# Kernel optimization log

Measured on AMD Instinct MI355X. Metric: run time of the kernel, lower is better.

## Reference

```python
import jax, jax.numpy as jnp
import numpy as np

B = 256; M = 6; H = 448; INC = 448; EMB = 32; NHEAD = 8; DFF = 2048
OBS = 20; HOR = 30
D = EMB + 4 * NHEAD + INC      # transformer d_model = 512 (requires INC == hidden_dim)
LBUF = OBS + HOR               # 50-token buffer; index 49 is written but never read
HD = D // NHEAD
FUS_IN = D + 7 + INC           # fusion layer input = 71 + 2*hidden_dim


def _ln(x, g, b):
    mu = x.mean(-1, keepdims=True)
    var = ((x - mu) ** 2).mean(-1, keepdims=True)
    return (x - mu) * jax.lax.rsqrt(var + 1e-5) * g + b


def setup_inputs() -> dict:
    key = jax.random.key(0)
    ks = jax.random.split(key, 16)
    s = jnp.float32(0.02)
    n = lambda i, shp: jax.random.normal(ks[i], shp, dtype=jnp.float32)
    return {
        "feat_in": n(0, (B, 1, INC)),
        "loc_in": n(1, (B, M, 2)),
        "obs_trajs": n(2, (OBS, B, 2)),
        "W_emb": n(3, (2, EMB)) * s, "b_emb": jnp.zeros((EMB,)),
        "W_qkv": n(4, (D, 3 * D)) * s, "b_qkv": jnp.zeros((3 * D,)),
        "W_o": n(5, (D, D)) * s, "b_o": jnp.zeros((D,)),
        "W_ff1": n(6, (D, DFF)) * s, "b_ff1": jnp.zeros((DFF,)),
        "W_ff2": n(7, (DFF, D)) * s, "b_ff2": jnp.zeros((D,)),
        "ln1_g": jnp.ones((D,)), "ln1_b": jnp.zeros((D,)),
        "ln2_g": jnp.ones((D,)), "ln2_b": jnp.zeros((D,)),
        "W_fus": n(8, (FUS_IN, H)) * s, "b_fus": jnp.zeros((H,)),
        "W_out": n(9, (H, 2)) * s, "b_out": jnp.zeros((2,)),
    }


def reference(feat_in, loc_in, obs_trajs, W_emb, b_emb, W_qkv, b_qkv, W_o, b_o,
              W_ff1, b_ff1, W_ff2, b_ff2, ln1_g, ln1_b, ln2_g, ln2_b,
              W_fus, b_fus, W_out, b_out):
    feat = feat_in[:, 0]                                     # [B, INC]
    emb_obs = jax.nn.relu(obs_trajs @ W_emb + b_emb)         # [OBS, B, EMB]
    pos0 = jnp.zeros((LBUF, B, 2), feat.dtype).at[:OBS].set(obs_trajs)
    emb0 = jnp.zeros((LBUF, B, EMB), feat.dtype).at[:OBS].set(emb_obs)
    idxs = jnp.arange(OBS, OBS + HOR)
    scale = 1.0 / jnp.sqrt(jnp.float32(HD))
    rep = NHEAD // 2

    def run_sample(goal):                                    # goal: [B, 2]
        def step(carry, frame_idx):
            pos, emb = carry
            last = pos[frame_idx - 1]                        # [B, 2]
            dist = goal - last
            tcol = jnp.zeros((B, 1), feat.dtype) + frame_idx
            # order matches torch.cat: (emb, goal, last, dist, time, feat)
            extras = jnp.concatenate([jnp.tile(goal, (1, rep)), jnp.tile(last, (1, rep)),
                                      jnp.tile(dist, (1, rep)), jnp.tile(tcol, (1, NHEAD))], -1)
            x = jnp.concatenate([emb,
                                 jnp.broadcast_to(extras, (LBUF, B, 4 * NHEAD)),
                                 jnp.broadcast_to(feat, (LBUF, B, INC))], -1)   # [LBUF, B, D]
            qkv = x @ W_qkv + b_qkv
            q, k, v = jnp.split(qkv, 3, axis=-1)
            qh = q[frame_idx - 1].reshape(B, NHEAD, HD)      # only last query needed
            kh = k.reshape(LBUF, B, NHEAD, HD)
            vh = v.reshape(LBUF, B, NHEAD, HD)
            scores = jnp.einsum('bhd,lbhd->bhl', qh, kh) * scale
            valid = jnp.arange(LBUF) < frame_idx             # tokens 0..frame_idx-1 exist
            scores = jnp.where(valid[None, None, :], scores, -1e9)
            attn = jax.nn.softmax(scores, axis=-1)
            ctx = jnp.einsum('bhl,lbhd->bhd', attn, vh).reshape(B, D)
            a = ctx @ W_o + b_o
            x_last = x[frame_idx - 1]
            h1 = _ln(x_last + a, ln1_g, ln1_b)               # post-LN encoder layer (eval, no dropout)
            ff = jax.nn.relu(h1 @ W_ff1 + b_ff1) @ W_ff2 + b_ff2
            h2 = _ln(h1 + ff, ln2_g, ln2_b)
            fus = jnp.concatenate([h2, last, goal, dist, tcol, feat], -1)       # [B, FUS_IN]
            out = (fus @ W_fus + b_fus) @ W_out + b_out                         # [B, 2]
            pos = pos.at[frame_idx].set(out)
            emb = emb.at[frame_idx].set(jax.nn.relu(out @ W_emb + b_emb))
            return (pos, emb), out
        _, ys = jax.lax.scan(step, (pos0, emb0), idxs)
        return ys                                            # [HOR, B, 2]

    ys = jax.vmap(run_sample, in_axes=1)(loc_in)             # [M, HOR, B, 2]
    return ys.transpose(2, 0, 1, 3).reshape(B, M, HOR * 2)
```

## Files before the change

kernel.cpp:

```cpp
#include <hip/hip_runtime.h>
#include <math.h>

#define B_   256
#define N_   1536
#define OBS_ 20
#define HOR_ 30

typedef __bf16 bf16;
typedef bf16  bf16x8 __attribute__((ext_vector_type(8)));
typedef float f32x4  __attribute__((ext_vector_type(4)));

__global__ __launch_bounds__(256) void gemm_k(
    const float* __restrict__ A, int lda,
    const float* __restrict__ Bw, int ldb,
    float* __restrict__ C, bf16* __restrict__ Cb, int ldc,
    int K, const float* __restrict__ colBias)
{
    __shared__ float As[16][68];
    __shared__ float Bs[16][68];
    const int tid = threadIdx.x;
    const int tx = tid & 15, ty = tid >> 4;
    const int n0 = blockIdx.y * 64, j0 = blockIdx.x * 64;
    float acc[4][4] = {};
    const int a_kk = tid & 15, a_nn0 = tid >> 4;
    const int b_jj = tid & 63, b_kk0 = tid >> 6;
    for (int k0 = 0; k0 < K; k0 += 16) {
#pragma unroll
        for (int i = 0; i < 4; i++) {
            int nn = a_nn0 + 16 * i;
            As[a_kk][nn] = (k0 + a_kk < K) ? A[(size_t)(n0 + nn) * lda + k0 + a_kk] : 0.f;
        }
#pragma unroll
        for (int i = 0; i < 4; i++) {
            int kk = b_kk0 + 4 * i;
            Bs[kk][b_jj] = (k0 + kk < K) ? Bw[(size_t)(k0 + kk) * ldb + j0 + b_jj] : 0.f;
        }
        __syncthreads();
#pragma unroll
        for (int kk = 0; kk < 16; kk++) {
            float4 av = *(const float4*)&As[kk][ty * 4];
            float4 bv = *(const float4*)&Bs[kk][tx * 4];
            float aa[4] = {av.x, av.y, av.z, av.w};
            float bb[4] = {bv.x, bv.y, bv.z, bv.w};
#pragma unroll
            for (int i = 0; i < 4; i++)
#pragma unroll
                for (int j = 0; j < 4; j++) acc[i][j] += aa[i] * bb[j];
        }
        __syncthreads();
    }
#pragma unroll
    for (int i = 0; i < 4; i++) {
        int n = n0 + ty * 4 + i;
#pragma unroll
        for (int j = 0; j < 4; j++) {
            int jj = j0 + tx * 4 + j;
            float v = acc[i][j];
            if (colBias) v += colBias[jj];
            if (C)  C[(size_t)n * ldc + jj] = v;
            if (Cb) Cb[(size_t)n * ldc + jj] = (bf16)v;
        }
    }
}

__global__ void pack_k(const float* __restrict__ srcF, const bf16* __restrict__ srcB,
                       int srcRows, int KC, int J, int lds, bf16* __restrict__ dst)
{
    int idx = blockIdx.x * 256 + threadIdx.x;
    int total = (J / 16) * KC * 64;
    if (idx >= total) return;
    int lane = idx & 63;
    int kc = (idx >> 6) % KC;
    int jg = idx / (64 * KC);
    int k0 = kc * 32 + (lane >> 4) * 8;
    int col = jg * 16 + (lane & 15);
    bf16x8 v;
#pragma unroll
    for (int i = 0; i < 8; i++) {
        int r = k0 + i;
        float x = 0.f;
        if (r < srcRows) x = srcF ? srcF[(size_t)r * lds + col] : (float)srcB[(size_t)r * lds + col];
        v[i] = (bf16)x;
    }
    *(bf16x8*)&dst[(size_t)idx * 8] = v;
}

template<int KC>
__global__ __launch_bounds__(256) void fgemm_k(
    const bf16* __restrict__ A, int lda,
    const bf16* __restrict__ Bp,
    float* __restrict__ C, bf16* __restrict__ Cb, int ldc,
    const float* __restrict__ colBias,
    const float* __restrict__ rowMat, int ldRm,
    int doRelu)
{
    const int n0 = blockIdx.y * 32;
    const int j0g = blockIdx.x * 4;
    const int tid = threadIdx.x;
    const int w = tid >> 6, lane = tid & 63;
    const int quad = lane >> 4, m15 = lane & 15;
    const int r0 = (w & 1) * 16;
    const int cg = (w >> 1) * 2;
    const bf16* Arow = &A[(size_t)(n0 + r0 + m15) * lda + quad * 8];
    const bf16* B0 = &Bp[((size_t)(j0g + cg) * KC * 64 + lane) * 8];
    const bf16* B1 = &Bp[((size_t)(j0g + cg + 1) * KC * 64 + lane) * 8];
    f32x4 acc0 = {}, acc1 = {};
#pragma unroll 8
    for (int kc = 0; kc < KC; kc++) {
        bf16x8 af = *(const bf16x8*)&Arow[kc * 32];
        bf16x8 b0 = *(const bf16x8*)&B0[(size_t)kc * 512];
        bf16x8 b1 = *(const bf16x8*)&B1[(size_t)kc * 512];
        acc0 = __builtin_amdgcn_mfma_f32_16x16x32_bf16(af, b0, acc0, 0, 0, 0);
        acc1 = __builtin_amdgcn_mfma_f32_16x16x32_bf16(af, b1, acc1, 0, 0, 0);
    }
#pragma unroll
    for (int g = 0; g < 2; g++) {
        f32x4 a = g ? acc1 : acc0;
        int j = (j0g + cg + g) * 16 + m15;
        float cb = colBias ? colBias[j] : 0.f;
#pragma unroll
        for (int r = 0; r < 4; r++) {
            int n = n0 + r0 + quad * 4 + r;
            float v = a[r] + cb;
            if (rowMat) v += rowMat[(size_t)(n / 6) * ldRm + j];
            if (doRelu) v = fmaxf(v, 0.f);
            if (C)  C[(size_t)n * ldc + j] = v;
            if (Cb) Cb[(size_t)n * ldc + j] = (bf16)v;
        }
    }
}

__global__ __launch_bounds__(256) void emb_obs_k(
    const float* __restrict__ obs, const float* __restrict__ Wemb,
    const float* __restrict__ bemb, float* __restrict__ emb_obs)
{
    int tid = blockIdx.x * 256 + threadIdx.x;
    if (tid >= OBS_ * B_ * 32) return;
    int r = tid >> 5, e = tid & 31;
    float v = obs[r * 2] * Wemb[e] + obs[r * 2 + 1] * Wemb[32 + e] + bemb[e];
    emb_obs[tid] = fmaxf(v, 0.f);
}

__global__ __launch_bounds__(256) void weff_k(
    const float* __restrict__ Wqkv, const float* __restrict__ bqkv,
    float* __restrict__ Weff)
{
    __shared__ float qrow[512];
    const int r = blockIdx.x;
    const int t = threadIdx.x;
    for (int j = t; j < 512; j += 256)
        qrow[j] = (r < 512) ? Wqkv[(size_t)r * 1536 + j] : bqkv[j];
    __syncthreads();
    const int h = t >> 5, c = t & 31;
    float acc = 0.f;
#pragma unroll 8
    for (int d = 0; d < 64; d++)
        acc += qrow[h * 64 + d] * Wqkv[(size_t)c * 1536 + 512 + h * 64 + d];
    Weff[(size_t)r * 256 + t] = acc;
}

__global__ __launch_bounds__(256) void wov_k(
    const float* __restrict__ Wqkv, const float* __restrict__ Wo,
    bf16* __restrict__ WovCat)
{
    __shared__ float vrow[64];
    const int row = blockIdx.x;
    const int h = row >> 5, c = row & 31;
    const int t = threadIdx.x;
    if (t < 64) vrow[t] = Wqkv[(size_t)c * 1536 + 1024 + h * 64 + t];
    __syncthreads();
    for (int j = t; j < 512; j += 256) {
        float acc = 0.f;
#pragma unroll 8
        for (int d = 0; d < 64; d++)
            acc += vrow[d] * Wo[(size_t)(h * 64 + d) * 512 + j];
        WovCat[(size_t)row * 512 + j] = (bf16)acc;
    }
}

__global__ __launch_bounds__(256) void attn_k(
    const float* __restrict__ qp, const float* __restrict__ emb_obs,
    const float* __restrict__ emb_gen, bf16* __restrict__ ecA1b, int t)
{
    __shared__ float qp_s[256];
    __shared__ float emb_s[50 * 33];
    __shared__ float at_s[4][64];
    const int n = blockIdx.x, b = n / 6, tid = threadIdx.x;
    qp_s[tid] = qp[(size_t)n * 256 + tid];
    for (int idx = tid; idx < t * 32; idx += 256) {
        int l = idx >> 5, c = idx & 31;
        emb_s[l * 33 + c] = (l < OBS_) ? emb_obs[((size_t)l * B_ + b) * 32 + c]
                                       : emb_gen[((size_t)(l - OBS_) * N_ + n) * 32 + c];
    }
    __syncthreads();
    const int w = tid >> 6, lane = tid & 63;
#pragma unroll
    for (int hh = 0; hh < 2; hh++) {
        const int h = w * 2 + hh;
        float sc = -1e30f;
        if (lane < t) {
            float s_ = 0.f;
#pragma unroll 8
            for (int c = 0; c < 32; c++) s_ += emb_s[lane * 33 + c] * qp_s[h * 32 + c];
            sc = s_ * 0.125f;
        }
        float mx = sc;
#pragma unroll
        for (int o = 32; o > 0; o >>= 1) mx = fmaxf(mx, __shfl_xor(mx, o, 64));
        float e = (lane < t) ? __expf(sc - mx) : 0.f;
        float sm = e;
#pragma unroll
        for (int o = 32; o > 0; o >>= 1) sm += __shfl_xor(sm, o, 64);
        at_s[w][lane] = e / sm;
        if (lane < 32) {
            float ec = 0.f;
            for (int l = 0; l < t; l++) ec += at_s[w][l] * emb_s[l * 33 + lane];
            ecA1b[(size_t)n * 288 + h * 32 + lane] = (bf16)ec;
        }
    }
}

__global__ __launch_bounds__(256) void ln1_k(
    const float* __restrict__ a, const float* __restrict__ A1f,
    const float* __restrict__ feat, const float* __restrict__ g,
    const float* __restrict__ bt, float* __restrict__ h1f, bf16* __restrict__ h1b)
{
    __shared__ float red[8];
    const int n = blockIdx.x, b = n / 6, tid = threadIdx.x;
    float r[2]; float s = 0.f, sq = 0.f;
#pragma unroll
    for (int i = 0; i < 2; i++) {
        int j = tid + i * 256;
        float x = (j < 64) ? A1f[(size_t)n * 64 + j] : feat[(size_t)b * 448 + (j - 64)];
        float v = a[(size_t)n * 512 + j] + x;
        r[i] = v; s += v; sq += v * v;
    }
#pragma unroll
    for (int o = 32; o > 0; o >>= 1) { s += __shfl_xor(s, o, 64); sq += __shfl_xor(sq, o, 64); }
    int w = tid >> 6, lane = tid & 63;
    if (lane == 0) { red[w] = s; red[4 + w] = sq; }
    __syncthreads();
    s  = red[0] + red[1] + red[2] + red[3];
    sq = red[4] + red[5] + red[6] + red[7];
    float mu = s * (1.f / 512.f);
    float var = sq * (1.f / 512.f) - mu * mu;
    float rs = rsqrtf(var + 1e-5f);
#pragma unroll
    for (int i = 0; i < 2; i++) {
        int j = tid + i * 256;
        float v = (r[i] - mu) * rs * g[j] + bt[j];
        h1f[(size_t)n * 512 + j] = v;
        h1b[(size_t)n * 512 + j] = (bf16)v;
    }
}

__global__ __launch_bounds__(256) void ln2_k(
    const float* __restrict__ h1, const float* __restrict__ ff,
    const float* __restrict__ g, const float* __restrict__ bt,
    const float* __restrict__ small5, bf16* __restrict__ h2p)
{
    __shared__ float red[8];
    const int n = blockIdx.x, tid = threadIdx.x;
    float r[2]; float s = 0.f, sq = 0.f;
#pragma unroll
    for (int i = 0; i < 2; i++) {
        int j = tid + i * 256;
        float v = h1[(size_t)n * 512 + j] + ff[(size_t)n * 512 + j];
        r[i] = v; s += v; sq += v * v;
    }
#pragma unroll
    for (int o = 32; o > 0; o >>= 1) { s += __shfl_xor(s, o, 64); sq += __shfl_xor(sq, o, 64); }
    int w = tid >> 6, lane = tid & 63;
    if (lane == 0) { red[w] = s; red[4 + w] = sq; }
    __syncthreads();
    s  = red[0] + red[1] + red[2] + red[3];
    sq = red[4] + red[5] + red[6] + red[7];
    float mu = s * (1.f / 512.f);
    float var = sq * (1.f / 512.f) - mu * mu;
    float rs = rsqrtf(var + 1e-5f);
#pragma unroll
    for (int i = 0; i < 2; i++) {
        int j = tid + i * 256;
        h2p[(size_t)n * 544 + j] = (bf16)((r[i] - mu) * rs * g[j] + bt[j]);
    }
    if (tid < 7)  h2p[(size_t)n * 544 + 512 + tid] = (bf16)small5[n * 8 + tid];
    if (tid < 25) h2p[(size_t)n * 544 + 519 + tid] = (bf16)0.f;
}

__device__ __forceinline__ void next_state(
    int n, int b, int t, float o0, float o1, float g0, float g1, float tc,
    const float* Wemb, const float* bemb, const float* Weff, const float* featqp,
    float* emb_dst, float* A1f, bf16* ecA1b, float* small5, float* qp, float* A1s)
{
    float d0 = g0 - o0, d1 = g1 - o1;
    if (t < 32) {
        float e = fmaxf(o0 * Wemb[t] + o1 * Wemb[32 + t] + bemb[t], 0.f);
        if (emb_dst) emb_dst[t] = e;
        A1s[t] = e;
    } else if (t < 64) {
        int c = t - 32;
        float v;
        if      (c < 8)  v = (c & 1) ? g1 : g0;
        else if (c < 16) v = (c & 1) ? o1 : o0;
        else if (c < 24) v = (c & 1) ? d1 : d0;
        else             v = tc;
        A1s[t] = v;
    }
    if (t < 7) {
        float v2 = (t==0)?o0:(t==1)?o1:(t==2)?g0:(t==3)?g1:(t==4)?d0:(t==5)?d1:tc;
        small5[n * 8 + t] = v2;
    }
    __syncthreads();
    if (t < 64) {
        A1f[(size_t)n * 64 + t] = A1s[t];
        if (t >= 32) ecA1b[(size_t)n * 288 + 256 + (t - 32)] = (bf16)A1s[t];
    }
    float acc = featqp[(size_t)b * 256 + t];
#pragma unroll 8
    for (int k = 0; k < 64; k++) acc += A1s[k] * Weff[k * 256 + t];
    qp[(size_t)n * 256 + t] = acc;
}

__global__ __launch_bounds__(256) void init_k(
    const float* __restrict__ obs, const float* __restrict__ emb_obs,
    const float* __restrict__ loc, const float* __restrict__ Weff,
    const float* __restrict__ featqp,
    float* __restrict__ A1f, bf16* __restrict__ ecA1b,
    float* __restrict__ small5, float* __restrict__ qp)
{
    __shared__ float A1s[64];
    const int n = blockIdx.x, b = n / 6, m = n % 6, t = threadIdx.x;
    float o0 = obs[(19 * B_ + b) * 2], o1 = obs[(19 * B_ + b) * 2 + 1];
    float g0 = loc[b * 12 + m * 2], g1 = loc[b * 12 + m * 2 + 1];
    if (t < 32) {
        A1s[t] = emb_obs[((size_t)19 * B_ + b) * 32 + t];
    } else if (t < 64) {
        int c = t - 32; float d0 = g0 - o0, d1 = g1 - o1; float tc = 20.f;
        float v;
        if      (c < 8)  v = (c & 1) ? g1 : g0;
        else if (c < 16) v = (c & 1) ? o1 : o0;
        else if (c < 24) v = (c & 1) ? d1 : d0;
        else             v = tc;
        A1s[t] = v;
    }
    if (t < 7) {
        float d0 = g0 - o0, d1 = g1 - o1; float tc = 20.f;
        float v2 = (t==0)?o0:(t==1)?o1:(t==2)?g0:(t==3)?g1:(t==4)?d0:(t==5)?d1:tc;
        small5[n * 8 + t] = v2;
    }
    __syncthreads();
    if (t < 64) {
        A1f[(size_t)n * 64 + t] = A1s[t];
        if (t >= 32) ecA1b[(size_t)n * 288 + 256 + (t - 32)] = (bf16)A1s[t];
    }
    float acc = featqp[(size_t)b * 256 + t];
#pragma unroll 8
    for (int k = 0; k < 64; k++) acc += A1s[k] * Weff[k * 256 + t];
    qp[(size_t)n * 256 + t] = acc;
}

__global__ __launch_bounds__(256) void finish_k(
    const float* __restrict__ fusv, const float* __restrict__ Wout,
    const float* __restrict__ bout, const float* __restrict__ Wemb,
    const float* __restrict__ bemb, const float* __restrict__ loc,
    const float* __restrict__ Weff, const float* __restrict__ featqp,
    float* __restrict__ dout, float* __restrict__ emb_gen,
    float* __restrict__ A1f, bf16* __restrict__ ecA1b,
    float* __restrict__ small5, float* __restrict__ qp, int s)
{
    __shared__ float red[8];
    __shared__ float osh[2];
    __shared__ float A1s[64];
    const int n = blockIdx.x, b = n / 6, m = n % 6, t = threadIdx.x;
    float f0 = fusv[(size_t)n * 448 + t];
    float p0 = f0 * Wout[t * 2];
    float p1 = f0 * Wout[t * 2 + 1];
    if (t < 192) {
        float f1 = fusv[(size_t)n * 448 + 256 + t];
        p0 += f1 * Wout[(256 + t) * 2];
        p1 += f1 * Wout[(256 + t) * 2 + 1];
    }
#pragma unroll
    for (int o = 32; o > 0; o >>= 1) { p0 += __shfl_xor(p0, o, 64); p1 += __shfl_xor(p1, o, 64); }
    int w = t >> 6, lane = t & 63;
    if (lane == 0) { red[w] = p0; red[4 + w] = p1; }
    __syncthreads();
    if (t == 0) {
        float o0 = red[0] + red[1] + red[2] + red[3] + bout[0];
        float o1 = red[4] + red[5] + red[6] + red[7] + bout[1];
        osh[0] = o0; osh[1] = o1;
        dout[(size_t)b * 360 + m * 60 + s * 2]     = o0;
        dout[(size_t)b * 360 + m * 60 + s * 2 + 1] = o1;
    }
    __syncthreads();
    float o0 = osh[0], o1 = osh[1];
    float g0 = loc[b * 12 + m * 2], g1 = loc[b * 12 + m * 2 + 1];
    next_state(n, b, t, o0, o1, g0, g1, (float)(OBS_ + s + 1),
               Wemb, bemb, Weff, featqp,
               &emb_gen[((size_t)s * N_ + n) * 32], A1f, ecA1b, small5, qp, A1s);
}

extern "C" void kernel_launch(void* const* d_in, const int* in_sizes, int n_in,
                              void* d_out_, int out_size, void* d_ws, size_t ws_size,
                              hipStream_t stream) {
    (void)in_sizes; (void)n_in; (void)out_size; (void)ws_size;
    const float* feat  = (const float*)d_in[0];
    const float* loc   = (const float*)d_in[1];
    const float* obs   = (const float*)d_in[2];
    const float* W_emb = (const float*)d_in[3];
    const float* b_emb = (const float*)d_in[4];
    const float* W_qkv = (const float*)d_in[5];
    const float* b_qkv = (const float*)d_in[6];
    const float* W_o   = (const float*)d_in[7];
    const float* b_o   = (const float*)d_in[8];
    const float* W_ff1 = (const float*)d_in[9];
    const float* b_ff1 = (const float*)d_in[10];
    const float* W_ff2 = (const float*)d_in[11];
    const float* b_ff2 = (const float*)d_in[12];
    const float* ln1_g = (const float*)d_in[13];
    const float* ln1_b = (const float*)d_in[14];
    const float* ln2_g = (const float*)d_in[15];
    const float* ln2_b = (const float*)d_in[16];
    const float* W_fus = (const float*)d_in[17];
    const float* b_fus = (const float*)d_in[18];
    const float* W_out = (const float*)d_in[19];
    const float* b_out = (const float*)d_in[20];
    float* dout = (float*)d_out_;

    float* ws = (float*)d_ws;
    float* Weff     = ws; ws += 513 * 256;
    float* featqp   = ws; ws += 256 * 256;
    float* featv    = ws; ws += 256 * 512;
    float* featvO   = ws; ws += 256 * 512;
    float* feat_fus = ws; ws += 256 * 448;
    float* emb_obs  = ws; ws += OBS_ * B_ * 32;
    float* emb_gen  = ws; ws += HOR_ * N_ * 32;
    float* qp       = ws; ws += (size_t)N_ * 256;
    float* A1f      = ws; ws += (size_t)N_ * 64;
    float* small5   = ws; ws += (size_t)N_ * 8;
    float* h1f      = ws; ws += (size_t)N_ * 512;
    float* aF       = ws; ws += (size_t)N_ * 512;
    float* ffB      = ws; ws += (size_t)N_ * 512;
    float* fusv     = ws; ws += (size_t)N_ * 448;
    bf16* WovCat = (bf16*)ws; ws += (320 * 512) / 2;
    bf16* BpA    = (bf16*)ws; ws += (32 * 9 * 512) / 2;
    bf16* BpF1   = (bf16*)ws; ws += (128 * 16 * 512) / 2;
    bf16* BpF2   = (bf16*)ws; ws += (32 * 64 * 512) / 2;
    bf16* BpFus  = (bf16*)ws; ws += (28 * 17 * 512) / 2;
    bf16* ecA1b  = (bf16*)ws; ws += ((size_t)N_ * 288) / 2;
    bf16* h1b    = (bf16*)ws; ws += ((size_t)N_ * 512) / 2;
    bf16* f1b    = (bf16*)ws; ws += ((size_t)N_ * 2048) / 2;
    bf16* h2p    = (bf16*)ws; ws += ((size_t)N_ * 544) / 2;

    emb_obs_k<<<dim3(640), dim3(256), 0, stream>>>(obs, W_emb, b_emb, emb_obs);
    weff_k<<<dim3(513), dim3(256), 0, stream>>>(W_qkv, b_qkv, Weff);
    gemm_k<<<dim3(4, 4), dim3(256), 0, stream>>>(feat, 448, Weff + 64 * 256, 256,
        featqp, nullptr, 256, 448, Weff + 512 * 256);
    wov_k<<<dim3(256), dim3(256), 0, stream>>>(W_qkv, W_o, WovCat);
    gemm_k<<<dim3(8, 4), dim3(256), 0, stream>>>(feat, 448, W_qkv + 64 * 1536 + 1024, 1536,
        featv, nullptr, 512, 448, b_qkv + 1024);
    gemm_k<<<dim3(8, 4), dim3(256), 0, stream>>>(featv, 512, W_o, 512,
        featvO, nullptr, 512, 512, b_o);
    gemm_k<<<dim3(8, 1), dim3(256), 0, stream>>>(W_qkv + 32 * 1536 + 1024, 1536, W_o, 512,
        featv, WovCat + 256 * 512, 512, 512, nullptr);
    gemm_k<<<dim3(7, 4), dim3(256), 0, stream>>>(feat, 448, W_fus + 519 * 448, 448,
        feat_fus, nullptr, 448, 448, b_fus);
    pack_k<<<dim3(72),  dim3(256), 0, stream>>>(nullptr, WovCat, 288, 9,  512,  512,  BpA);
    pack_k<<<dim3(512), dim3(256), 0, stream>>>(W_ff1, nullptr, 512, 16, 2048, 2048, BpF1);
    pack_k<<<dim3(512), dim3(256), 0, stream>>>(W_ff2, nullptr, 2048, 64, 512, 512,  BpF2);
    pack_k<<<dim3(120), dim3(256), 0, stream>>>(W_fus, nullptr, 519, 17, 448,  448,  BpFus);
    init_k<<<dim3(N_), dim3(256), 0, stream>>>(obs, emb_obs, loc, Weff, featqp,
        A1f, ecA1b, small5, qp);

    for (int s = 0; s < HOR_; s++) {
        attn_k<<<dim3(N_), dim3(256), 0, stream>>>(qp, emb_obs, emb_gen, ecA1b, OBS_ + s);
        fgemm_k<9><<<dim3(8, 48), dim3(256), 0, stream>>>(ecA1b, 288, BpA,
            aF, nullptr, 512, nullptr, featvO, 512, 0);
        ln1_k<<<dim3(N_), dim3(256), 0, stream>>>(aF, A1f, feat, ln1_g, ln1_b, h1f, h1b);
        fgemm_k<16><<<dim3(32, 48), dim3(256), 0, stream>>>(h1b, 512, BpF1,
            nullptr, f1b, 2048, b_ff1, nullptr, 0, 1);
        fgemm_k<64><<<dim3(8, 48), dim3(256), 0, stream>>>(f1b, 2048, BpF2,
            ffB, nullptr, 512, b_ff2, nullptr, 0, 0);
        ln2_k<<<dim3(N_), dim3(256), 0, stream>>>(h1f, ffB, ln2_g, ln2_b, small5, h2p);
        fgemm_k<17><<<dim3(7, 48), dim3(256), 0, stream>>>(h2p, 544, BpFus,
            fusv, nullptr, 448, nullptr, feat_fus, 448, 0);
        finish_k<<<dim3(N_), dim3(256), 0, stream>>>(fusv, W_out, b_out, W_emb, b_emb,
            loc, Weff, featqp, dout, emb_gen, A1f, ecA1b, small5, qp, s);
    }
}
```

Before: 2.938 ms.

## Fuse layernorms into neighbouring MFMA GEMMs and residual adds into epilogues

```diff
diff --git a/kernel.cpp b/kernel.cpp
--- a/kernel.cpp
+++ b/kernel.cpp
@@ -9,6 +9,10 @@
 typedef __bf16 bf16;
 typedef bf16  bf16x8 __attribute__((ext_vector_type(8)));
 typedef float f32x4  __attribute__((ext_vector_type(4)));
+
+__device__ __forceinline__ f32x4 MF(bf16x8 a, bf16x8 b, f32x4 c) {
+    return __builtin_amdgcn_mfma_f32_16x16x32_bf16(a, b, c, 0, 0, 0);
+}
 
 __global__ __launch_bounds__(256) void gemm_k(
     const float* __restrict__ A, int lda,
@@ -85,51 +89,6 @@
     *(bf16x8*)&dst[(size_t)idx * 8] = v;
 }
 
-template<int KC>
-__global__ __launch_bounds__(256) void fgemm_k(
-    const bf16* __restrict__ A, int lda,
-    const bf16* __restrict__ Bp,
-    float* __restrict__ C, bf16* __restrict__ Cb, int ldc,
-    const float* __restrict__ colBias,
-    const float* __restrict__ rowMat, int ldRm,
-    int doRelu)
-{
-    const int n0 = blockIdx.y * 32;
-    const int j0g = blockIdx.x * 4;
-    const int tid = threadIdx.x;
-    const int w = tid >> 6, lane = tid & 63;
-    const int quad = lane >> 4, m15 = lane & 15;
-    const int r0 = (w & 1) * 16;
-    const int cg = (w >> 1) * 2;
-    const bf16* Arow = &A[(size_t)(n0 + r0 + m15) * lda + quad * 8];
-    const bf16* B0 = &Bp[((size_t)(j0g + cg) * KC * 64 + lane) * 8];
-    const bf16* B1 = &Bp[((size_t)(j0g + cg + 1) * KC * 64 + lane) * 8];
-    f32x4 acc0 = {}, acc1 = {};
-#pragma unroll 8
-    for (int kc = 0; kc < KC; kc++) {
-        bf16x8 af = *(const bf16x8*)&Arow[kc * 32];
-        bf16x8 b0 = *(const bf16x8*)&B0[(size_t)kc * 512];
-        bf16x8 b1 = *(const bf16x8*)&B1[(size_t)kc * 512];
-        acc0 = __builtin_amdgcn_mfma_f32_16x16x32_bf16(af, b0, acc0, 0, 0, 0);
-        acc1 = __builtin_amdgcn_mfma_f32_16x16x32_bf16(af, b1, acc1, 0, 0, 0);
-    }
-#pragma unroll
-    for (int g = 0; g < 2; g++) {
-        f32x4 a = g ? acc1 : acc0;
-        int j = (j0g + cg + g) * 16 + m15;
-        float cb = colBias ? colBias[j] : 0.f;
-#pragma unroll
-        for (int r = 0; r < 4; r++) {
-            int n = n0 + r0 + quad * 4 + r;
-            float v = a[r] + cb;
-            if (rowMat) v += rowMat[(size_t)(n / 6) * ldRm + j];
-            if (doRelu) v = fmaxf(v, 0.f);
-            if (C)  C[(size_t)n * ldc + j] = v;
-            if (Cb) Cb[(size_t)n * ldc + j] = (bf16)v;
-        }
-    }
-}
-
 __global__ __launch_bounds__(256) void emb_obs_k(
     const float* __restrict__ obs, const float* __restrict__ Wemb,
     const float* __restrict__ bemb, float* __restrict__ emb_obs)
@@ -176,149 +135,6 @@
             acc += vrow[d] * Wo[(size_t)(h * 64 + d) * 512 + j];
         WovCat[(size_t)row * 512 + j] = (bf16)acc;
     }
-}
-
-__global__ __launch_bounds__(256) void attn_k(
-    const float* __restrict__ qp, const float* __restrict__ emb_obs,
-    const float* __restrict__ emb_gen, bf16* __restrict__ ecA1b, int t)
-{
-    __shared__ float qp_s[256];
-    __shared__ float emb_s[50 * 33];
-    __shared__ float at_s[4][64];
-    const int n = blockIdx.x, b = n / 6, tid = threadIdx.x;
-    qp_s[tid] = qp[(size_t)n * 256 + tid];
-    for (int idx = tid; idx < t * 32; idx += 256) {
-        int l = idx >> 5, c = idx & 31;
-        emb_s[l * 33 + c] = (l < OBS_) ? emb_obs[((size_t)l * B_ + b) * 32 + c]
-                                       : emb_gen[((size_t)(l - OBS_) * N_ + n) * 32 + c];
-    }
-    __syncthreads();
-    const int w = tid >> 6, lane = tid & 63;
-#pragma unroll
-    for (int hh = 0; hh < 2; hh++) {
-        const int h = w * 2 + hh;
-        float sc = -1e30f;
-        if (lane < t) {
-            float s_ = 0.f;
-#pragma unroll 8
-            for (int c = 0; c < 32; c++) s_ += emb_s[lane * 33 + c] * qp_s[h * 32 + c];
-            sc = s_ * 0.125f;
-        }
-        float mx = sc;
-#pragma unroll
-        for (int o = 32; o > 0; o >>= 1) mx = fmaxf(mx, __shfl_xor(mx, o, 64));
-        float e = (lane < t) ? __expf(sc - mx) : 0.f;
-        float sm = e;
-#pragma unroll
-        for (int o = 32; o > 0; o >>= 1) sm += __shfl_xor(sm, o, 64);
-        at_s[w][lane] = e / sm;
-        if (lane < 32) {
-            float ec = 0.f;
-            for (int l = 0; l < t; l++) ec += at_s[w][l] * emb_s[l * 33 + lane];
-            ecA1b[(size_t)n * 288 + h * 32 + lane] = (bf16)ec;
-        }
-    }
-}
-
-__global__ __launch_bounds__(256) void ln1_k(
-    const float* __restrict__ a, const float* __restrict__ A1f,
-    const float* __restrict__ feat, const float* __restrict__ g,
-    const float* __restrict__ bt, float* __restrict__ h1f, bf16* __restrict__ h1b)
-{
-    __shared__ float red[8];
-    const int n = blockIdx.x, b = n / 6, tid = threadIdx.x;
-    float r[2]; float s = 0.f, sq = 0.f;
-#pragma unroll
-    for (int i = 0; i < 2; i++) {
-        int j = tid + i * 256;
-        float x = (j < 64) ? A1f[(size_t)n * 64 + j] : feat[(size_t)b * 448 + (j - 64)];
-        float v = a[(size_t)n * 512 + j] + x;
-        r[i] = v; s += v; sq += v * v;
-    }
-#pragma unroll
-    for (int o = 32; o > 0; o >>= 1) { s += __shfl_xor(s, o, 64); sq += __shfl_xor(sq, o, 64); }
-    int w = tid >> 6, lane = tid & 63;
-    if (lane == 0) { red[w] = s; red[4 + w] = sq; }
-    __syncthreads();
-    s  = red[0] + red[1] + red[2] + red[3];
-    sq = red[4] + red[5] + red[6] + red[7];
-    float mu = s * (1.f / 512.f);
-    float var = sq * (1.f / 512.f) - mu * mu;
-    float rs = rsqrtf(var + 1e-5f);
-#pragma unroll
-    for (int i = 0; i < 2; i++) {
-        int j = tid + i * 256;
-        float v = (r[i] - mu) * rs * g[j] + bt[j];
-        h1f[(size_t)n * 512 + j] = v;
-        h1b[(size_t)n * 512 + j] = (bf16)v;
-    }
-}
-
-__global__ __launch_bounds__(256) void ln2_k(
-    const float* __restrict__ h1, const float* __restrict__ ff,
-    const float* __restrict__ g, const float* __restrict__ bt,
-    const float* __restrict__ small5, bf16* __restrict__ h2p)
-{
-    __shared__ float red[8];
-    const int n = blockIdx.x, tid = threadIdx.x;
-    float r[2]; float s = 0.f, sq = 0.f;
-#pragma unroll
-    for (int i = 0; i < 2; i++) {
-        int j = tid + i * 256;
-        float v = h1[(size_t)n * 512 + j] + ff[(size_t)n * 512 + j];
-        r[i] = v; s += v; sq += v * v;
-    }
-#pragma unroll
-    for (int o = 32; o > 0; o >>= 1) { s += __shfl_xor(s, o, 64); sq += __shfl_xor(sq, o, 64); }
-    int w = tid >> 6, lane = tid & 63;
-    if (lane == 0) { red[w] = s; red[4 + w] = sq; }
-    __syncthreads();
-    s  = red[0] + red[1] + red[2] + red[3];
-    sq = red[4] + red[5] + red[6] + red[7];
-    float mu = s * (1.f / 512.f);
-    float var = sq * (1.f / 512.f) - mu * mu;
-    float rs = rsqrtf(var + 1e-5f);
-#pragma unroll
-    for (int i = 0; i < 2; i++) {
-        int j = tid + i * 256;
-        h2p[(size_t)n * 544 + j] = (bf16)((r[i] - mu) * rs * g[j] + bt[j]);
-    }
-    if (tid < 7)  h2p[(size_t)n * 544 + 512 + tid] = (bf16)small5[n * 8 + tid];
-    if (tid < 25) h2p[(size_t)n * 544 + 519 + tid] = (bf16)0.f;
-}
-
-__device__ __forceinline__ void next_state(
-    int n, int b, int t, float o0, float o1, float g0, float g1, float tc,
-    const float* Wemb, const float* bemb, const float* Weff, const float* featqp,
-    float* emb_dst, float* A1f, bf16* ecA1b, float* small5, float* qp, float* A1s)
-{
-    float d0 = g0 - o0, d1 = g1 - o1;
-    if (t < 32) {
-        float e = fmaxf(o0 * Wemb[t] + o1 * Wemb[32 + t] + bemb[t], 0.f);
-        if (emb_dst) emb_dst[t] = e;
-        A1s[t] = e;
-    } else if (t < 64) {
-        int c = t - 32;
-        float v;
-        if      (c < 8)  v = (c & 1) ? g1 : g0;
-        else if (c < 16) v = (c & 1) ? o1 : o0;
-        else if (c < 24) v = (c & 1) ? d1 : d0;
-        else             v = tc;
-        A1s[t] = v;
-    }
-    if (t < 7) {
-        float v2 = (t==0)?o0:(t==1)?o1:(t==2)?g0:(t==3)?g1:(t==4)?d0:(t==5)?d1:tc;
-        small5[n * 8 + t] = v2;
-    }
-    __syncthreads();
-    if (t < 64) {
-        A1f[(size_t)n * 64 + t] = A1s[t];
-        if (t >= 32) ecA1b[(size_t)n * 288 + 256 + (t - 32)] = (bf16)A1s[t];
-    }
-    float acc = featqp[(size_t)b * 256 + t];
-#pragma unroll 8
-    for (int k = 0; k < 64; k++) acc += A1s[k] * Weff[k * 256 + t];
-    qp[(size_t)n * 256 + t] = acc;
 }
 
 __global__ __launch_bounds__(256) void init_k(
@@ -345,6 +161,309 @@
     }
     if (t < 7) {
         float d0 = g0 - o0, d1 = g1 - o1; float tc = 20.f;
+        float v2 = (t==0)?o0:(t==1)?o1:(t==2)?g0:(t==3)?g1:(t==4)?d0:(t==5)?d1:tc;
+        small5[n * 8 + t] = v2;
+    }
+    __syncthreads();
+    if (t < 64) {
+        A1f[(size_t)n * 64 + t] = A1s[t];
+        if (t >= 32) ecA1b[(size_t)n * 288 + 256 + (t - 32)] = (bf16)A1s[t];
+    }
+    float acc = featqp[(size_t)b * 256 + t];
+#pragma unroll 8
+    for (int k = 0; k < 64; k++) acc += A1s[k] * Weff[k * 256 + t];
+    qp[(size_t)n * 256 + t] = acc;
+}
+
+__global__ __launch_bounds__(256) void attn_k(
+    const float* __restrict__ qp, const float* __restrict__ emb_obs,
+    const float* __restrict__ emb_gen, bf16* __restrict__ ecA1b, int t)
+{
+    __shared__ float qp_s[256];
+    __shared__ float emb_s[50 * 33];
+    __shared__ float at_s[4][64];
+    const int n = blockIdx.x, b = n / 6, tid = threadIdx.x;
+    qp_s[tid] = qp[(size_t)n * 256 + tid];
+    for (int idx = tid; idx < t * 32; idx += 256) {
+        int l = idx >> 5, c = idx & 31;
+        emb_s[l * 33 + c] = (l < OBS_) ? emb_obs[((size_t)l * B_ + b) * 32 + c]
+                                       : emb_gen[((size_t)(l - OBS_) * N_ + n) * 32 + c];
+    }
+    __syncthreads();
+    const int w = tid >> 6, lane = tid & 63;
+#pragma unroll
+    for (int hh = 0; hh < 2; hh++) {
+        const int h = w * 2 + hh;
+        float sc = -1e30f;
+        if (lane < t) {
+            float s_ = 0.f;
+#pragma unroll 8
+            for (int c = 0; c < 32; c++) s_ += emb_s[lane * 33 + c] * qp_s[h * 32 + c];
+            sc = s_ * 0.125f;
+        }
+        float mx = sc;
+#pragma unroll
+        for (int o = 32; o > 0; o >>= 1) mx = fmaxf(mx, __shfl_xor(mx, o, 64));
+        float e = (lane < t) ? __expf(sc - mx) : 0.f;
+        float sm = e;
+#pragma unroll
+        for (int o = 32; o > 0; o >>= 1) sm += __shfl_xor(sm, o, 64);
+        at_s[w][lane] = e / sm;
+        if (lane < 32) {
+            float ec = 0.f;
+            for (int l = 0; l < t; l++) ec += at_s[w][l] * emb_s[l * 33 + lane];
+            ecA1b[(size_t)n * 288 + h * 32 + lane] = (bf16)ec;
+        }
+    }
+}
+
+__global__ __launch_bounds__(256) void agemm_k(
+    const bf16* __restrict__ A, const bf16* __restrict__ Bp,
+    const float* __restrict__ featvO, const float* __restrict__ A1f,
+    const float* __restrict__ feat, float* __restrict__ aF)
+{
+    const int n0 = blockIdx.y * 32;
+    const int j0g = blockIdx.x * 4;
+    const int tid = threadIdx.x;
+    const int w = tid >> 6, lane = tid & 63;
+    const int quad = lane >> 4, m15 = lane & 15;
+    const int r0 = (w & 1) * 16;
+    const int cg = (w >> 1) * 2;
+    const bf16* Arow = &A[(size_t)(n0 + r0 + m15) * 288 + quad * 8];
+    const bf16* B0 = &Bp[((size_t)(j0g + cg) * 9 * 64 + lane) * 8];
+    const bf16* B1 = &Bp[((size_t)(j0g + cg + 1) * 9 * 64 + lane) * 8];
+    f32x4 a0 = {}, a1 = {};
+#pragma unroll
+    for (int kc = 0; kc < 9; kc++) {
+        bf16x8 af = *(const bf16x8*)&Arow[kc * 32];
+        bf16x8 b0 = *(const bf16x8*)&B0[(size_t)kc * 512];
+        bf16x8 b1 = *(const bf16x8*)&B1[(size_t)kc * 512];
+        a0 = MF(af, b0, a0); a1 = MF(af, b1, a1);
+    }
+#pragma unroll
+    for (int g = 0; g < 2; g++) {
+        f32x4 ac = g ? a1 : a0;
+        int j = (j0g + cg + g) * 16 + m15;
+#pragma unroll
+        for (int r = 0; r < 4; r++) {
+            int n = n0 + r0 + quad * 4 + r, b = n / 6;
+            float x = (j < 64) ? A1f[(size_t)n * 64 + j] : feat[(size_t)b * 448 + (j - 64)];
+            aF[(size_t)n * 512 + j] = ac[r] + featvO[(size_t)b * 512 + j] + x;
+        }
+    }
+}
+
+__global__ __launch_bounds__(256) void ff1ln_k(
+    const float* __restrict__ aF, const bf16* __restrict__ Bp,
+    const float* __restrict__ g1, const float* __restrict__ b1,
+    const float* __restrict__ bff1,
+    bf16* __restrict__ f1b, float* __restrict__ h1f)
+{
+    __shared__ bf16 frag[2 * 16 * 64 * 8];
+    __shared__ float mu_s[32], rs_s[32];
+    const int n0 = blockIdx.y * 32;
+    const int jb = blockIdx.x;
+    const int tid = threadIdx.x;
+    const int w = tid >> 6, lane = tid & 63;
+    const int quad = lane >> 4, m15 = lane & 15;
+
+    {
+        int row = tid >> 3, part = tid & 7;
+        const float* base = &aF[(size_t)(n0 + row) * 512 + part * 64];
+        float s = 0.f, sq = 0.f;
+#pragma unroll
+        for (int i = 0; i < 16; i++) {
+            float4 v = *(const float4*)&base[i * 4];
+            s += v.x + v.y + v.z + v.w;
+            sq += v.x * v.x + v.y * v.y + v.z * v.z + v.w * v.w;
+        }
+#pragma unroll
+        for (int o = 1; o < 8; o <<= 1) { s += __shfl_xor(s, o, 64); sq += __shfl_xor(sq, o, 64); }
+        if (part == 0) {
+            float mu = s * (1.f / 512.f);
+            float var = sq * (1.f / 512.f) - mu * mu;
+            mu_s[row] = mu; rs_s[row] = rsqrtf(var + 1e-5f);
+        }
+    }
+    __syncthreads();
+#pragma unroll
+    for (int it = 0; it < 8; it++) {
+        int q = tid + it * 256;
+        int ln = q & 63, kc = (q >> 6) & 15, rg = q >> 10;
+        int row = rg * 16 + (ln & 15), k0 = kc * 32 + (ln >> 4) * 8;
+        const float* src = &aF[(size_t)(n0 + row) * 512 + k0];
+        float mu = mu_s[row], rs = rs_s[row];
+        float fo[8]; bf16x8 v8;
+#pragma unroll
+        for (int i = 0; i < 8; i++) {
+            fo[i] = (src[i] - mu) * rs * g1[k0 + i] + b1[k0 + i];
+            v8[i] = (bf16)fo[i];
+        }
+        *(bf16x8*)&frag[((size_t)(rg * 16 + kc) * 64 + ln) * 8] = v8;
+        if (jb == 0) {
+            float4 o0 = {fo[0], fo[1], fo[2], fo[3]}, o1 = {fo[4], fo[5], fo[6], fo[7]};
+            *(float4*)&h1f[(size_t)(n0 + row) * 512 + k0]     = o0;
+            *(float4*)&h1f[(size_t)(n0 + row) * 512 + k0 + 4] = o1;
+        }
+    }
+    __syncthreads();
+    {
+        const int jgA = jb * 8 + w * 2, jgB = jgA + 1;
+        const bf16* B0 = &Bp[((size_t)jgA * 16 * 64 + lane) * 8];
+        const bf16* B1 = &Bp[((size_t)jgB * 16 * 64 + lane) * 8];
+        f32x4 a00 = {}, a01 = {}, a10 = {}, a11 = {};
+#pragma unroll
+        for (int kc = 0; kc < 16; kc++) {
+            bf16x8 fa0 = *(const bf16x8*)&frag[((size_t)kc * 64 + lane) * 8];
+            bf16x8 fa1 = *(const bf16x8*)&frag[((size_t)(16 + kc) * 64 + lane) * 8];
+            bf16x8 b0 = *(const bf16x8*)&B0[(size_t)kc * 512];
+            bf16x8 b1 = *(const bf16x8*)&B1[(size_t)kc * 512];
+            a00 = MF(fa0, b0, a00); a01 = MF(fa0, b1, a01);
+            a10 = MF(fa1, b0, a10); a11 = MF(fa1, b1, a11);
+        }
+        float cb0 = bff1[jgA * 16 + m15], cb1 = bff1[jgB * 16 + m15];
+#pragma unroll
+        for (int r = 0; r < 4; r++) {
+            int na = n0 + quad * 4 + r, nb = n0 + 16 + quad * 4 + r;
+            f1b[(size_t)na * 2048 + jgA * 16 + m15] = (bf16)fmaxf(a00[r] + cb0, 0.f);
+            f1b[(size_t)na * 2048 + jgB * 16 + m15] = (bf16)fmaxf(a01[r] + cb1, 0.f);
+            f1b[(size_t)nb * 2048 + jgA * 16 + m15] = (bf16)fmaxf(a10[r] + cb0, 0.f);
+            f1b[(size_t)nb * 2048 + jgB * 16 + m15] = (bf16)fmaxf(a11[r] + cb1, 0.f);
+        }
+    }
+}
+
+__global__ __launch_bounds__(256) void ff2_k(
+    const bf16* __restrict__ A, const bf16* __restrict__ Bp,
+    const float* __restrict__ bff2, const float* __restrict__ h1f,
+    float* __restrict__ ffa)
+{
+    const int n0 = blockIdx.y * 32;
+    const int j0g = blockIdx.x * 4;
+    const int tid = threadIdx.x;
+    const int w = tid >> 6, lane = tid & 63;
+    const int quad = lane >> 4, m15 = lane & 15;
+    const int r0 = (w & 1) * 16;
+    const int cg = (w >> 1) * 2;
+    const bf16* Arow = &A[(size_t)(n0 + r0 + m15) * 2048 + quad * 8];
+    const bf16* B0 = &Bp[((size_t)(j0g + cg) * 64 * 64 + lane) * 8];
+    const bf16* B1 = &Bp[((size_t)(j0g + cg + 1) * 64 * 64 + lane) * 8];
+    f32x4 a0 = {}, a1 = {};
+#pragma unroll 8
+    for (int kc = 0; kc < 64; kc++) {
+        bf16x8 af = *(const bf16x8*)&Arow[kc * 32];
+        bf16x8 b0 = *(const bf16x8*)&B0[(size_t)kc * 512];
+        bf16x8 b1 = *(const bf16x8*)&B1[(size_t)kc * 512];
+        a0 = MF(af, b0, a0); a1 = MF(af, b1, a1);
+    }
+#pragma unroll
+    for (int g = 0; g < 2; g++) {
+        f32x4 ac = g ? a1 : a0;
+        int j = (j0g + cg + g) * 16 + m15;
+        float cb = bff2[j];
+#pragma unroll
+        for (int r = 0; r < 4; r++) {
+            int n = n0 + r0 + quad * 4 + r;
+            ffa[(size_t)n * 512 + j] = ac[r] + cb + h1f[(size_t)n * 512 + j];
+        }
+    }
+}
+
+__global__ __launch_bounds__(256) void fusln_k(
+    const float* __restrict__ ffa, const bf16* __restrict__ Bp,
+    const float* __restrict__ g2, const float* __restrict__ b2,
+    const float* __restrict__ small5, const float* __restrict__ feat_fus,
+    float* __restrict__ fusv)
+{
+    __shared__ bf16 frag[2 * 17 * 64 * 8];
+    __shared__ float mu_s[32], rs_s[32];
+    const int n0 = blockIdx.y * 32;
+    const int jb = blockIdx.x;
+    const int tid = threadIdx.x;
+    const int w = tid >> 6, lane = tid & 63;
+    const int quad = lane >> 4, m15 = lane & 15;
+
+    {
+        int row = tid >> 3, part = tid & 7;
+        const float* base = &ffa[(size_t)(n0 + row) * 512 + part * 64];
+        float s = 0.f, sq = 0.f;
+#pragma unroll
+        for (int i = 0; i < 16; i++) {
+            float4 v = *(const float4*)&base[i * 4];
+            s += v.x + v.y + v.z + v.w;
+            sq += v.x * v.x + v.y * v.y + v.z * v.z + v.w * v.w;
+        }
+#pragma unroll
+        for (int o = 1; o < 8; o <<= 1) { s += __shfl_xor(s, o, 64); sq += __shfl_xor(sq, o, 64); }
+        if (part == 0) {
+            float mu = s * (1.f / 512.f);
+            float var = sq * (1.f / 512.f) - mu * mu;
+            mu_s[row] = mu; rs_s[row] = rsqrtf(var + 1e-5f);
+        }
+    }
+    __syncthreads();
+    for (int it = 0; it < 9; it++) {
+        int q = tid + it * 256;
+        if (q < 2176) {
+            int ln = q & 63, kc = (q >> 6) % 17, rg = q / (64 * 17);
+            int row = rg * 16 + (ln & 15), k0 = kc * 32 + (ln >> 4) * 8;
+            int n = n0 + row;
+            float mu = mu_s[row], rs = rs_s[row];
+            bf16x8 v8;
+#pragma unroll
+            for (int i = 0; i < 8; i++) {
+                int k = k0 + i;
+                float val;
+                if (k < 512)      val = (ffa[(size_t)n * 512 + k] - mu) * rs * g2[k] + b2[k];
+                else if (k < 519) val = small5[(size_t)n * 8 + (k - 512)];
+                else              val = 0.f;
+                v8[i] = (bf16)val;
+            }
+            *(bf16x8*)&frag[((size_t)(rg * 17 + kc) * 64 + ln) * 8] = v8;
+        }
+    }
+    __syncthreads();
+    {
+        const int jg = jb * 4 + w;
+        const bf16* B0 = &Bp[((size_t)jg * 17 * 64 + lane) * 8];
+        f32x4 a0 = {}, a1 = {};
+#pragma unroll
+        for (int kc = 0; kc < 17; kc++) {
+            bf16x8 fa0 = *(const bf16x8*)&frag[((size_t)kc * 64 + lane) * 8];
+            bf16x8 fa1 = *(const bf16x8*)&frag[((size_t)(17 + kc) * 64 + lane) * 8];
+            bf16x8 b0 = *(const bf16x8*)&B0[(size_t)kc * 512];
+            a0 = MF(fa0, b0, a0); a1 = MF(fa1, b0, a1);
+        }
+        int j = jg * 16 + m15;
+#pragma unroll
+        for (int r = 0; r < 4; r++) {
+            int na = n0 + quad * 4 + r, nb = n0 + 16 + quad * 4 + r;
+            fusv[(size_t)na * 448 + j] = a0[r] + feat_fus[(size_t)(na / 6) * 448 + j];
+            fusv[(size_t)nb * 448 + j] = a1[r] + feat_fus[(size_t)(nb / 6) * 448 + j];
+        }
+    }
+}
+
+__device__ __forceinline__ void next_state(
+    int n, int b, int t, float o0, float o1, float g0, float g1, float tc,
+    const float* Wemb, const float* bemb, const float* Weff, const float* featqp,
+    float* emb_dst, float* A1f, bf16* ecA1b, float* small5, float* qp, float* A1s)
+{
+    float d0 = g0 - o0, d1 = g1 - o1;
+    if (t < 32) {
+        float e = fmaxf(o0 * Wemb[t] + o1 * Wemb[32 + t] + bemb[t], 0.f);
+        if (emb_dst) emb_dst[t] = e;
+        A1s[t] = e;
+    } else if (t < 64) {
+        int c = t - 32;
+        float v;
+        if      (c < 8)  v = (c & 1) ? g1 : g0;
+        else if (c < 16) v = (c & 1) ? o1 : o0;
+        else if (c < 24) v = (c & 1) ? d1 : d0;
+        else             v = tc;
+        A1s[t] = v;
+    }
+    if (t < 7) {
         float v2 = (t==0)?o0:(t==1)?o1:(t==2)?g0:(t==3)?g1:(t==4)?d0:(t==5)?d1:tc;
         small5[n * 8 + t] = v2;
     }
@@ -440,7 +559,7 @@
     float* small5   = ws; ws += (size_t)N_ * 8;
     float* h1f      = ws; ws += (size_t)N_ * 512;
     float* aF       = ws; ws += (size_t)N_ * 512;
-    float* ffB      = ws; ws += (size_t)N_ * 512;
+    float* ffa      = ws; ws += (size_t)N_ * 512;
     float* fusv     = ws; ws += (size_t)N_ * 448;
     bf16* WovCat = (bf16*)ws; ws += (320 * 512) / 2;
     bf16* BpA    = (bf16*)ws; ws += (32 * 9 * 512) / 2;
@@ -448,9 +567,7 @@
     bf16* BpF2   = (bf16*)ws; ws += (32 * 64 * 512) / 2;
     bf16* BpFus  = (bf16*)ws; ws += (28 * 17 * 512) / 2;
     bf16* ecA1b  = (bf16*)ws; ws += ((size_t)N_ * 288) / 2;
-    bf16* h1b    = (bf16*)ws; ws += ((size_t)N_ * 512) / 2;
     bf16* f1b    = (bf16*)ws; ws += ((size_t)N_ * 2048) / 2;
-    bf16* h2p    = (bf16*)ws; ws += ((size_t)N_ * 544) / 2;
 
     emb_obs_k<<<dim3(640), dim3(256), 0, stream>>>(obs, W_emb, b_emb, emb_obs);
     weff_k<<<dim3(513), dim3(256), 0, stream>>>(W_qkv, b_qkv, Weff);
@@ -474,16 +591,10 @@
 
     for (int s = 0; s < HOR_; s++) {
         attn_k<<<dim3(N_), dim3(256), 0, stream>>>(qp, emb_obs, emb_gen, ecA1b, OBS_ + s);
-        fgemm_k<9><<<dim3(8, 48), dim3(256), 0, stream>>>(ecA1b, 288, BpA,
-            aF, nullptr, 512, nullptr, featvO, 512, 0);
-        ln1_k<<<dim3(N_), dim3(256), 0, stream>>>(aF, A1f, feat, ln1_g, ln1_b, h1f, h1b);
-        fgemm_k<16><<<dim3(32, 48), dim3(256), 0, stream>>>(h1b, 512, BpF1,
-            nullptr, f1b, 2048, b_ff1, nullptr, 0, 1);
-        fgemm_k<64><<<dim3(8, 48), dim3(256), 0, stream>>>(f1b, 2048, BpF2,
-            ffB, nullptr, 512, b_ff2, nullptr, 0, 0);
-        ln2_k<<<dim3(N_), dim3(256), 0, stream>>>(h1f, ffB, ln2_g, ln2_b, small5, h2p);
-        fgemm_k<17><<<dim3(7, 48), dim3(256), 0, stream>>>(h2p, 544, BpFus,
-            fusv, nullptr, 448, nullptr, feat_fus, 448, 0);
+        agemm_k<<<dim3(8, 48), dim3(256), 0, stream>>>(ecA1b, BpA, featvO, A1f, feat, aF);
+        ff1ln_k<<<dim3(16, 48), dim3(256), 0, stream>>>(aF, BpF1, ln1_g, ln1_b, b_ff1, f1b, h1f);
+        ff2_k<<<dim3(8, 48), dim3(256), 0, stream>>>(f1b, BpF2, b_ff2, h1f, ffa);
+        fusln_k<<<dim3(7, 48), dim3(256), 0, stream>>>(ffa, BpFus, ln2_g, ln2_b, small5, feat_fus, fusv);
         finish_k<<<dim3(N_), dim3(256), 0, stream>>>(fusv, W_out, b_out, W_emb, b_emb,
             loc, Weff, featqp, dout, emb_gen, A1f, ecA1b, small5, qp, s);
     }
```

New measurement: 3.319 ms. 13.0% more time.
